# Kernel optimization log

Hardware: AMD Instinct MI355X
Metric: run time of the kernel (lower is better)

## Reference

```python
import jax, jax.numpy as jnp
import numpy as np


def _conv(x, w, padding):
    # x: (N,H,W,Cin), w: (kh,kw,Cin,Cout)
    return jax.lax.conv_general_dilated(x, w, (1, 1), padding,
                                        dimension_numbers=('NHWC', 'HWIO', 'NHWC'))


def _hard_sigmoid(x):
    # Keras default recurrent_activation for ConvLSTM2D
    return jnp.clip(0.2 * x + 0.5, 0.0, 1.0)


def _convlstm(x, Wx, Wh, b):
    # x: (B,T,H,W,Cin); Wx: (3,3,Cin,4F) input conv (VALID, as Keras padding default);
    # Wh: (3,3,F,4F) recurrent conv (SAME, Keras always); b: (4F,). Gate order i,f,c,o.
    B, T, H, W, C = x.shape
    F = Wh.shape[2]
    # Input convolutions are state-independent: compute for all timesteps at once.
    xg = _conv(x.reshape(B * T, H, W, C), Wx, 'VALID') + b  # (B*T, H-2, W-2, 4F)
    Ho, Wo = xg.shape[1], xg.shape[2]
    xg = xg.reshape(B, T, Ho, Wo, 4 * F).transpose(1, 0, 2, 3, 4)  # (T,B,Ho,Wo,4F)
    h0 = jnp.zeros((B, Ho, Wo, F), x.dtype)

    def step(carry, g_t):
        h, c = carry
        g = g_t + _conv(h, Wh, 'SAME')
        i, f, cc, o = jnp.split(g, 4, axis=-1)
        c = _hard_sigmoid(f) * c + _hard_sigmoid(i) * jnp.tanh(cc)
        h = _hard_sigmoid(o) * jnp.tanh(c)
        return (h, c), h

    _, hs = jax.lax.scan(step, (h0, h0), xg)  # hs: (T,B,Ho,Wo,F)
    return hs.transpose(1, 0, 2, 3, 4)


def _maxpool_hw(x):
    # MaxPooling3D pool=(1,2,2), stride=pool, padding='same' on (B,T,H,W,C)
    return jax.lax.reduce_window(x, -jnp.inf, jax.lax.max,
                                 (1, 1, 2, 2, 1), (1, 1, 2, 2, 1), 'SAME')


def setup_inputs() -> dict:
    key = jax.random.key(0)
    ks = jax.random.split(key, 11)
    B, T, H, W, C = 32, 24, 128, 128, 3
    NUM_CLASSES = 50
    FLAT = 24 * 7 * 7 * 16  # = 18816, see shape trace
    p = lambda k, s: (jax.random.normal(k, s, jnp.float32) * 0.05)
    return {
        'x': jax.random.normal(ks[0], (B, T, H, W, C), jnp.float32),
        'Wx1': p(ks[1], (3, 3, 3, 16)),  'Wh1': p(ks[2], (3, 3, 4, 16)),  'b1': jnp.zeros((16,), jnp.float32),
        'Wx2': p(ks[3], (3, 3, 4, 32)),  'Wh2': p(ks[4], (3, 3, 8, 32)),  'b2': jnp.zeros((32,), jnp.float32),
        'Wx3': p(ks[5], (3, 3, 8, 48)),  'Wh3': p(ks[6], (3, 3, 12, 48)), 'b3': jnp.zeros((48,), jnp.float32),
        'Wx4': p(ks[7], (3, 3, 12, 64)), 'Wh4': p(ks[8], (3, 3, 16, 64)), 'b4': jnp.zeros((64,), jnp.float32),
        'Wd': p(ks[9], (FLAT, NUM_CLASSES)), 'bd': jnp.zeros((NUM_CLASSES,), jnp.float32),
    }


def reference(x, Wx1, Wh1, b1, Wx2, Wh2, b2, Wx3, Wh3, b3, Wx4, Wh4, b4, Wd, bd):
    # Dropout layers are identity at inference.
    x = _maxpool_hw(_convlstm(x, Wx1, Wh1, b1))
    x = _maxpool_hw(_convlstm(x, Wx2, Wh2, b2))
    x = _maxpool_hw(_convlstm(x, Wx3, Wh3, b3))
    x = _maxpool_hw(_convlstm(x, Wx4, Wh4, b4))
    x = x.reshape(x.shape[0], -1)  # Keras Flatten: row-major over (T,H,W,C)
    return jax.nn.softmax(x @ Wd + bd, axis=-1)
```

## Files before the change

kernel.cpp:

```cpp
#include <hip/hip_runtime.h>
#include <math.h>


static __device__ __forceinline__ float hsig(float x) {
    return fminf(fmaxf(fmaf(0.2f, x, 0.5f), 0.0f), 1.0f);
}
static __device__ __forceinline__ float ftanh(float x) {
    float e = __builtin_amdgcn_exp2f(x * 2.88539008177792681f);
    return 1.0f - 2.0f * __builtin_amdgcn_rcpf(e + 1.0f);
}

constexpr int H1SL = 32 * 126 * 126 * 4;
constexpr int H2SL = 32 * 61 * 61 * 8;
constexpr int H3SL = 32 * 29 * 29 * 12;
constexpr int H4SL = 32 * 13 * 13 * 16;
constexpr size_t O_H1 = 0;
constexpr size_t O_H2 = O_H1 + 2 * (size_t)H1SL;
constexpr size_t O_H3 = O_H2 + 2 * (size_t)H2SL;
constexpr size_t O_H4 = O_H3 + 2 * (size_t)H3SL;
constexpr size_t O_C1 = O_H4 + 2 * (size_t)H4SL;
constexpr size_t O_C2 = O_C1 + (size_t)H1SL;
constexpr size_t O_C3 = O_C2 + (size_t)H2SL;
constexpr size_t O_C4 = O_C3 + (size_t)H3SL;
constexpr size_t O_P1 = O_C4 + (size_t)H4SL;
constexpr size_t O_P2 = O_P1 + (size_t)(768 * 63 * 63 * 4);
constexpr size_t O_P3 = O_P2 + (size_t)(768 * 31 * 31 * 8);
constexpr size_t O_P4 = O_P3 + (size_t)(768 * 15 * 15 * 12);
constexpr size_t O_DP = O_P4 + (size_t)(768 * 7 * 7 * 16);

__host__ __device__ static inline int role_blocks(int r, int s) {
    int t;
    switch (r) {
    case 0: t = s - 8; return (t >= 0 && t < 24) ? 32   : 0;
    case 1: t = s - 6; return (t >= 0 && t < 24) ? 85   : 0;
    case 2: t = s - 4; return (t >= 0 && t < 24) ? 421  : 0;
    case 3: t = s;     return (t >= 0 && t < 24) ? 993  : 0;
    case 4: t = s - 2; return (t >= 0 && t < 24) ? 1861 : 0;
    case 5: t = s - 1; return (t >= 0 && t < 24) ? 497  : 0;
    case 6: t = s - 3; return (t >= 0 && t < 24) ? 121  : 0;
    case 7: t = s - 5; return (t >= 0 && t < 24) ? 29   : 0;
    case 8: t = s - 7; return (t >= 0 && t < 24) ? 7    : 0;
    }
    return 0;
}
constexpr int NSTAGES = 32;

__device__ __forceinline__
void step_pair_d(const float* __restrict__ P,
                 const float* __restrict__ Wx,
                 const float* __restrict__ Wh,
                 const float* __restrict__ bias,
                 const float* __restrict__ h_prev,
                 float* __restrict__ h_cur,
                 float* __restrict__ cbuf,
                 int t, int lb)
{
    constexpr int CIN = 3, F = 4, HIN = 128, WIN = 128;
    constexpr int B = 32, T = 24, HO = 126, WO = 126, G = 16;
    constexpr int XP = WO / 2;
    constexpr int NPAIR = B * HO * XP;
    const int id = lb * 256 + (int)threadIdx.x;
    if (id >= NPAIR) return;
    const int xp = id % XP;
    const int yy = (id / XP) % HO;
    const int b  = id / (XP * HO);
    const int x0 = 2 * xp;

    float acc[2][4][F];
    #pragma unroll
    for (int u = 0; u < 2; ++u)
        #pragma unroll
        for (int g = 0; g < 4; ++g)
            #pragma unroll
            for (int f = 0; f < F; ++f)
                acc[u][g][f] = bias[g * F + f];

    const float* Pt = P + (size_t)(b * T + t) * HIN * WIN * CIN;
    #pragma unroll
    for (int ky = 0; ky < 3; ++ky) {
        const float* prow = Pt + ((size_t)(yy + ky) * WIN + x0) * CIN;
        float pv[4 * CIN];
        #pragma unroll
        for (int j = 0; j < 2 * CIN; ++j) {
            float2 v2 = reinterpret_cast<const float2*>(prow)[j];
            pv[2 * j] = v2.x; pv[2 * j + 1] = v2.y;
        }
        #pragma unroll
        for (int dx = 0; dx < 4; ++dx)
            #pragma unroll
            for (int ci = 0; ci < CIN; ++ci) {
                const float v = pv[dx * CIN + ci];
                #pragma unroll
                for (int u = 0; u < 2; ++u) {
                    const int kx = dx - u;
                    if (kx >= 0 && kx <= 2) {
                        const float* wr =
                            Wx + (size_t)((ky * 3 + kx) * CIN + ci) * G;
                        #pragma unroll
                        for (int g = 0; g < 4; ++g)
                            #pragma unroll
                            for (int f = 0; f < F; ++f)
                                acc[u][g][f] = fmaf(v, wr[g * F + f], acc[u][g][f]);
                    }
                }
            }
    }

    if (t > 0) {
        #pragma unroll
        for (int ky = 0; ky < 3; ++ky) {
            const int hy = yy + ky - 1;
            if (hy < 0 || hy >= HO) continue;
            const float* hrow = h_prev + ((size_t)b * HO + hy) * WO * F;
            #pragma unroll
            for (int dx = 0; dx < 4; ++dx) {
                const int hx = x0 - 1 + dx;
                if (dx == 0 && x0 == 0) continue;
                if (dx == 3 && hx >= WO) continue;
                const float4* h4 =
                    reinterpret_cast<const float4*>(hrow + (size_t)hx * F);
                float hv[F];
                #pragma unroll
                for (int j = 0; j < F / 4; ++j) {
                    float4 v4 = h4[j];
                    hv[4*j] = v4.x; hv[4*j+1] = v4.y;
                    hv[4*j+2] = v4.z; hv[4*j+3] = v4.w;
                }
                #pragma unroll
                for (int ci = 0; ci < F; ++ci) {
                    const float v = hv[ci];
                    #pragma unroll
                    for (int u = 0; u < 2; ++u) {
                        const int kx = dx - u;
                        if (kx >= 0 && kx <= 2) {
                            const float* wr =
                                Wh + (size_t)((ky * 3 + kx) * F + ci) * G;
                            #pragma unroll
                            for (int g = 0; g < 4; ++g)
                                #pragma unroll
                                for (int f = 0; f < F; ++f)
                                    acc[u][g][f] =
                                        fmaf(v, wr[g * F + f], acc[u][g][f]);
                        }
                    }
                }
            }
        }
    }

    #pragma unroll
    for (int u = 0; u < 2; ++u) {
        const size_t pix = ((size_t)b * HO + yy) * WO + (x0 + u);
        float cn[F], ho[F];
        float* cp = cbuf + pix * F;
        #pragma unroll
        for (int j = 0; j < F / 4; ++j) {
            float4 c4 = (t > 0) ? reinterpret_cast<float4*>(cp)[j]
                                : make_float4(0.f, 0.f, 0.f, 0.f);
            float cold[4] = {c4.x, c4.y, c4.z, c4.w};
            #pragma unroll
            for (int v = 0; v < 4; ++v) {
                const int f = 4 * j + v;
                const float ig = hsig(acc[u][0][f]), fg = hsig(acc[u][1][f]);
                const float cc = ftanh(acc[u][2][f]), og = hsig(acc[u][3][f]);
                cn[f] = fmaf(fg, cold[v], ig * cc);
                ho[f] = og * ftanh(cn[f]);
            }
            reinterpret_cast<float4*>(cp)[j] =
                make_float4(cn[4*j], cn[4*j+1], cn[4*j+2], cn[4*j+3]);
        }
        float* hp = h_cur + pix * F;
        #pragma unroll
        for (int j = 0; j < F / 4; ++j)
            reinterpret_cast<float4*>(hp)[j] =
                make_float4(ho[4*j], ho[4*j+1], ho[4*j+2], ho[4*j+3]);
    }
}

template<int CIN, int F, int HIN, int WIN>
__device__ __forceinline__
void step_split_d(const float* __restrict__ P,
                  const float* __restrict__ Wx,
                  const float* __restrict__ Wh,
                  const float* __restrict__ bias,
                  const float* __restrict__ h_prev,
                  float* __restrict__ h_cur,
                  float* __restrict__ cbuf,
                  int t, int lb, float* __restrict__ gb)
{
    constexpr int B = 32, T = 24, HO = HIN - 2, WO = WIN - 2, G = 4 * F;
    constexpr int NPIX = B * HO * WO;
    const int tid = (int)threadIdx.x, lane = tid & 63;
    const int w = __builtin_amdgcn_readfirstlane(tid >> 6);
    const int pix = lb * 64 + lane;
    const int pp  = (pix < NPIX) ? pix : NPIX - 1;
    const int sp  = pp % (HO * WO);
    const int b   = pp / (HO * WO);
    const int xx  = sp % WO, yy = sp / WO;

    float acc[F];
    #pragma unroll
    for (int f = 0; f < F; ++f) acc[f] = bias[w * F + f];

    const float* Pt = P + (size_t)(b * T + t) * HIN * WIN * CIN;
    #pragma unroll
    for (int ky = 0; ky < 3; ++ky) {
        #pragma unroll
        for (int kx = 0; kx < 3; ++kx) {
            const float* prow = Pt + ((size_t)(yy + ky) * WIN + (xx + kx)) * CIN;
            float pv[CIN];
            #pragma unroll
            for (int j = 0; j < CIN / 4; ++j) {
                float4 v4 = reinterpret_cast<const float4*>(prow)[j];
                pv[4*j] = v4.x; pv[4*j+1] = v4.y; pv[4*j+2] = v4.z; pv[4*j+3] = v4.w;
            }
            #pragma unroll
            for (int ci = 0; ci < CIN; ++ci) {
                const float v = pv[ci];
                const float* wr = Wx + (size_t)((ky * 3 + kx) * CIN + ci) * G + w * F;
                #pragma unroll
                for (int f = 0; f < F; ++f)
                    acc[f] = fmaf(v, wr[f], acc[f]);
            }
        }
    }

    if (t > 0) {
        const float* Hp = h_prev + (size_t)b * HO * WO * F;
        #pragma unroll
        for (int ky = 0; ky < 3; ++ky) {
            const int hy = yy + ky - 1;
            if (hy < 0 || hy >= HO) continue;
            #pragma unroll
            for (int kx = 0; kx < 3; ++kx) {
                const int hx = xx + kx - 1;
                if (hx < 0 || hx >= WO) continue;
                const float4* h4 = reinterpret_cast<const float4*>(
                    Hp + ((size_t)hy * WO + hx) * F);
                float hv[F];
                #pragma unroll
                for (int j = 0; j < F / 4; ++j) {
                    float4 v4 = h4[j];
                    hv[4*j] = v4.x; hv[4*j+1] = v4.y; hv[4*j+2] = v4.z; hv[4*j+3] = v4.w;
                }
                #pragma unroll
                for (int ci = 0; ci < F; ++ci) {
                    const float v = hv[ci];
                    const float* wr = Wh + (size_t)((ky * 3 + kx) * F + ci) * G + w * F;
                    #pragma unroll
                    for (int f = 0; f < F; ++f)
                        acc[f] = fmaf(v, wr[f], acc[f]);
                }
            }
        }
    }

    #pragma unroll
    for (int f = 0; f < F; ++f) gb[w * (64 * F) + lane * F + f] = acc[f];
    __syncthreads();

    #pragma unroll
    for (int r2 = 0; r2 < F / 4; ++r2) {
        const int it = r2 * 256 + tid;
        const int pl = it / F, fo = it % F;
        const int pix2 = lb * 64 + pl;
        if (pix2 < NPIX) {
            const float ig = hsig(gb[0 * (64*F) + it]), fg = hsig(gb[1 * (64*F) + it]);
            const float cc = ftanh(gb[2 * (64*F) + it]), og = hsig(gb[3 * (64*F) + it]);
            const size_t cix = (size_t)pix2 * F + fo;
            const float cold = (t > 0) ? cbuf[cix] : 0.0f;
            const float cnw = fmaf(fg, cold, ig * cc);
            cbuf[cix] = cnw;
            h_cur[cix] = og * ftanh(cnw);
        }
    }
}

template<int C, int H, int W, int HP, int WP>
__device__ __forceinline__
void pool_slice_d(const float* __restrict__ h,
                  float* __restrict__ outF,
                  int t, int lb)
{
    constexpr int B = 32, T = 24;
    const int idx = lb * 256 + (int)threadIdx.x;
    if (idx >= B * HP * WP) return;
    const int xo = idx % WP;
    const int yo = (idx / WP) % HP;
    const int b  = idx / (WP * HP);
    const int y0 = 2 * yo, x0 = 2 * xo;
    const float* p = h + ((size_t)(b * H + y0) * W + x0) * C;
    float m[C];
    #pragma unroll
    for (int j = 0; j < C / 4; ++j) {
        float4 v = reinterpret_cast<const float4*>(p)[j];
        m[4*j] = v.x; m[4*j+1] = v.y; m[4*j+2] = v.z; m[4*j+3] = v.w;
    }
    if (x0 + 1 < W) {
        const float4* q = reinterpret_cast<const float4*>(p + C);
        #pragma unroll
        for (int j = 0; j < C / 4; ++j) {
            float4 v = q[j];
            m[4*j]   = fmaxf(m[4*j],   v.x); m[4*j+1] = fmaxf(m[4*j+1], v.y);
            m[4*j+2] = fmaxf(m[4*j+2], v.z); m[4*j+3] = fmaxf(m[4*j+3], v.w);
        }
    }
    if (y0 + 1 < H) {
        const float4* q = reinterpret_cast<const float4*>(p + (size_t)W * C);
        #pragma unroll
        for (int j = 0; j < C / 4; ++j) {
            float4 v = q[j];
            m[4*j]   = fmaxf(m[4*j],   v.x); m[4*j+1] = fmaxf(m[4*j+1], v.y);
            m[4*j+2] = fmaxf(m[4*j+2], v.z); m[4*j+3] = fmaxf(m[4*j+3], v.w);
        }
        if (x0 + 1 < W) {
            const float4* q2 = reinterpret_cast<const float4*>(p + (size_t)(W + 1) * C);
            #pragma unroll
            for (int j = 0; j < C / 4; ++j) {
                float4 v = q2[j];
                m[4*j]   = fmaxf(m[4*j],   v.x); m[4*j+1] = fmaxf(m[4*j+1], v.y);
                m[4*j+2] = fmaxf(m[4*j+2], v.z); m[4*j+3] = fmaxf(m[4*j+3], v.w);
            }
        }
    }
    float* o = outF + ((size_t)(b * T + t) * HP * WP + (size_t)yo * WP + xo) * C;
    #pragma unroll
    for (int j = 0; j < C / 4; ++j)
        reinterpret_cast<float4*>(o)[j] =
            make_float4(m[4*j], m[4*j+1], m[4*j+2], m[4*j+3]);
}

__device__ __forceinline__
void dense_partial_d(const float* __restrict__ X, const float* __restrict__ Wd,
                     float* __restrict__ part, int ch, int lb,
                     float* __restrict__ red)
{
    constexpr int FLAT = 18816, K = 50, NC = 24, CHUNK = FLAT / NC;
    const int b = lb;
    const int tid = (int)threadIdx.x, lane = tid & 63, wv = tid >> 6;
    const float* xp = X + (size_t)b * FLAT;
    const int i0 = ch * CHUNK + wv * (CHUNK / 4);
    float a0 = 0.f, a1 = 0.f, a2 = 0.f, a3 = 0.f;
    if (lane < K) {
        #pragma unroll 4
        for (int i = i0; i < i0 + CHUNK / 4; i += 4) {
            a0 = fmaf(xp[i + 0], Wd[(size_t)(i + 0) * K + lane], a0);
            a1 = fmaf(xp[i + 1], Wd[(size_t)(i + 1) * K + lane], a1);
            a2 = fmaf(xp[i + 2], Wd[(size_t)(i + 2) * K + lane], a2);
            a3 = fmaf(xp[i + 3], Wd[(size_t)(i + 3) * K + lane], a3);
        }
    }
    red[tid] = (a0 + a1) + (a2 + a3);
    __syncthreads();
    if (tid < 64 && lane < K)
        part[((size_t)b * NC + ch) * K + lane]
            = red[tid] + red[tid + 64] + red[tid + 128] + red[tid + 192];
}

__global__ __launch_bounds__(256)
void pipe_k(const float* __restrict__ x,
            const float* __restrict__ Wx1, const float* __restrict__ Wh1, const float* __restrict__ b1,
            const float* __restrict__ Wx2, const float* __restrict__ Wh2, const float* __restrict__ b2,
            const float* __restrict__ Wx3, const float* __restrict__ Wh3, const float* __restrict__ b3,
            const float* __restrict__ Wx4, const float* __restrict__ Wh4, const float* __restrict__ b4,
            const float* __restrict__ Wd,
            float* __restrict__ ws, int s)
{
    float* h1 = ws + O_H1;  float* h2 = ws + O_H2;
    float* h3 = ws + O_H3;  float* h4 = ws + O_H4;
    float* c1 = ws + O_C1;  float* c2 = ws + O_C2;
    float* c3 = ws + O_C3;  float* c4 = ws + O_C4;
    float* p1 = ws + O_P1;  float* p2 = ws + O_P2;
    float* p3 = ws + O_P3;  float* p4 = ws + O_P4;
    float* dp = ws + O_DP;

    __shared__ float gb[4 * 64 * 16];

    int bid = (int)blockIdx.x, r = 0, cum = 0;
    for (; r < 9; ++r) {
        int n = role_blocks(r, s);
        if (bid < cum + n) break;
        cum += n;
    }
    const int lb = bid - cum;

    switch (r) {
    case 0: { const int ch = s - 8;
        dense_partial_d(p4, Wd, dp, ch, lb, gb); } break;
    case 1: { const int t = s - 6;
        step_split_d<12, 16, 15, 15>(p3, Wx4, Wh4, b4,
            h4 + ((t - 1) & 1) * (size_t)H4SL, h4 + (t & 1) * (size_t)H4SL,
            c4, t, lb, gb); } break;
    case 2: { const int t = s - 4;
        step_split_d<8, 12, 31, 31>(p2, Wx3, Wh3, b3,
            h3 + ((t - 1) & 1) * (size_t)H3SL, h3 + (t & 1) * (size_t)H3SL,
            c3, t, lb, gb); } break;
    case 3: { const int t = s;
        step_pair_d(x, Wx1, Wh1, b1,
            h1 + ((t - 1) & 1) * (size_t)H1SL, h1 + (t & 1) * (size_t)H1SL,
            c1, t, lb); } break;
    case 4: { const int t = s - 2;
        step_split_d<4, 8, 63, 63>(p1, Wx2, Wh2, b2,
            h2 + ((t - 1) & 1) * (size_t)H2SL, h2 + (t & 1) * (size_t)H2SL,
            c2, t, lb, gb); } break;
    case 5: { const int t = s - 1;
        pool_slice_d<4, 126, 126, 63, 63>(h1 + (t & 1) * (size_t)H1SL, p1, t, lb); } break;
    case 6: { const int t = s - 3;
        pool_slice_d<8, 61, 61, 31, 31>(h2 + (t & 1) * (size_t)H2SL, p2, t, lb); } break;
    case 7: { const int t = s - 5;
        pool_slice_d<12, 29, 29, 15, 15>(h3 + (t & 1) * (size_t)H3SL, p3, t, lb); } break;
    case 8: { const int t = s - 7;
        pool_slice_d<16, 13, 13, 7, 7>(h4 + (t & 1) * (size_t)H4SL, p4, t, lb); } break;
    }
}

__global__ __launch_bounds__(64)
void dense_finish_k(const float* __restrict__ part, const float* __restrict__ bd,
                    float* __restrict__ out)
{
    constexpr int K = 50, NC = 24;
    const int b = blockIdx.x, lane = threadIdx.x;
    float v = -INFINITY;
    if (lane < K) {
        v = bd[lane];
        #pragma unroll
        for (int c = 0; c < NC; ++c)
            v += part[((size_t)b * NC + c) * K + lane];
    }
    float m = v;
    #pragma unroll
    for (int off = 32; off > 0; off >>= 1) m = fmaxf(m, __shfl_xor(m, off));
    float e = (lane < K) ? __expf(v - m) : 0.0f;
    float sgm = e;
    #pragma unroll
    for (int off = 32; off > 0; off >>= 1) sgm += __shfl_xor(sgm, off);
    if (lane < K) out[(size_t)b * K + lane] = e / sgm;
}

extern "C" void kernel_launch(void* const* d_in, const int* in_sizes, int n_in,
                              void* d_out, int out_size, void* d_ws, size_t ws_size,
                              hipStream_t stream)
{
    const float* x   = (const float*)d_in[0];
    const float* Wx1 = (const float*)d_in[1];
    const float* Wh1 = (const float*)d_in[2];
    const float* b1  = (const float*)d_in[3];
    const float* Wx2 = (const float*)d_in[4];
    const float* Wh2 = (const float*)d_in[5];
    const float* b2  = (const float*)d_in[6];
    const float* Wx3 = (const float*)d_in[7];
    const float* Wh3 = (const float*)d_in[8];
    const float* b3  = (const float*)d_in[9];
    const float* Wx4 = (const float*)d_in[10];
    const float* Wh4 = (const float*)d_in[11];
    const float* b4  = (const float*)d_in[12];
    const float* Wd  = (const float*)d_in[13];
    const float* bd  = (const float*)d_in[14];
    float* out = (float*)d_out;
    float* ws  = (float*)d_ws;

    for (int s = 0; s < NSTAGES; ++s) {
        int nb = 0;
        for (int r = 0; r < 9; ++r) nb += role_blocks(r, s);
        pipe_k<<<nb, 256, 0, stream>>>(x,
                                       Wx1, Wh1, b1, Wx2, Wh2, b2,
                                       Wx3, Wh3, b3, Wx4, Wh4, b4,
                                       Wd, ws, s);
    }
    dense_finish_k<<<32, 64, 0, stream>>>(ws + O_DP, bd, out);
}
```

Measured before the change: 1.179 ms.

## Fuse max-pooling into ConvLSTM steps via atomic float max and shorten pipeline

```diff
diff --git a/kernel.cpp b/kernel.cpp
--- a/kernel.cpp
+++ b/kernel.cpp
@@ -8,6 +8,12 @@
 static __device__ __forceinline__ float ftanh(float x) {
     float e = __builtin_amdgcn_exp2f(x * 2.88539008177792681f);
     return 1.0f - 2.0f * __builtin_amdgcn_rcpf(e + 1.0f);
+}
+
+static __device__ __forceinline__ void atomic_fmax(float* a, float v) {
+    if (__float_as_uint(v) == 0x80000000u) v = 0.0f;
+    if (v >= 0.0f) atomicMax((int*)a, __float_as_int(v));
+    else           atomicMin((unsigned int*)a, __float_as_uint(v));
 }
 
 constexpr int H1SL = 32 * 126 * 126 * 4;
@@ -27,23 +33,30 @@
 constexpr size_t O_P3 = O_P2 + (size_t)(768 * 31 * 31 * 8);
 constexpr size_t O_P4 = O_P3 + (size_t)(768 * 15 * 15 * 12);
 constexpr size_t O_DP = O_P4 + (size_t)(768 * 7 * 7 * 16);
+constexpr size_t NPOOLF = O_DP - O_P1;
 
 __host__ __device__ static inline int role_blocks(int r, int s) {
     int t;
     switch (r) {
-    case 0: t = s - 8; return (t >= 0 && t < 24) ? 32   : 0;
-    case 1: t = s - 6; return (t >= 0 && t < 24) ? 85   : 0;
-    case 2: t = s - 4; return (t >= 0 && t < 24) ? 421  : 0;
+    case 0: t = s - 4; return (t >= 0 && t < 24) ? 32   : 0;
+    case 1: t = s - 3; return (t >= 0 && t < 24) ? 85   : 0;
+    case 2: t = s - 2; return (t >= 0 && t < 24) ? 421  : 0;
     case 3: t = s;     return (t >= 0 && t < 24) ? 993  : 0;
-    case 4: t = s - 2; return (t >= 0 && t < 24) ? 1861 : 0;
-    case 5: t = s - 1; return (t >= 0 && t < 24) ? 497  : 0;
-    case 6: t = s - 3; return (t >= 0 && t < 24) ? 121  : 0;
-    case 7: t = s - 5; return (t >= 0 && t < 24) ? 29   : 0;
-    case 8: t = s - 7; return (t >= 0 && t < 24) ? 7    : 0;
+    case 4: t = s - 1; return (t >= 0 && t < 24) ? 1861 : 0;
     }
     return 0;
 }
-constexpr int NSTAGES = 32;
+constexpr int NSTAGES = 28;
+
+__global__ __launch_bounds__(256)
+void init_pools_k(float* __restrict__ p)
+{
+    const size_t stride = (size_t)gridDim.x * 256 * 4;
+    for (size_t i = ((size_t)blockIdx.x * 256 + threadIdx.x) * 4;
+         i + 3 < NPOOLF; i += stride)
+        *reinterpret_cast<float4*>(p + i) =
+            make_float4(-INFINITY, -INFINITY, -INFINITY, -INFINITY);
+}
 
 __device__ __forceinline__
 void step_pair_d(const float* __restrict__ P,
@@ -53,6 +66,7 @@
                  const float* __restrict__ h_prev,
                  float* __restrict__ h_cur,
                  float* __restrict__ cbuf,
+                 float* __restrict__ pool,
                  int t, int lb)
 {
     constexpr int CIN = 3, F = 4, HIN = 128, WIN = 128;
@@ -148,10 +162,11 @@
         }
     }
 
+    float hov[2][F];
     #pragma unroll
     for (int u = 0; u < 2; ++u) {
         const size_t pix = ((size_t)b * HO + yy) * WO + (x0 + u);
-        float cn[F], ho[F];
+        float cn[F];
         float* cp = cbuf + pix * F;
         #pragma unroll
         for (int j = 0; j < F / 4; ++j) {
@@ -164,7 +179,7 @@
                 const float ig = hsig(acc[u][0][f]), fg = hsig(acc[u][1][f]);
                 const float cc = ftanh(acc[u][2][f]), og = hsig(acc[u][3][f]);
                 cn[f] = fmaf(fg, cold[v], ig * cc);
-                ho[f] = og * ftanh(cn[f]);
+                hov[u][f] = og * ftanh(cn[f]);
             }
             reinterpret_cast<float4*>(cp)[j] =
                 make_float4(cn[4*j], cn[4*j+1], cn[4*j+2], cn[4*j+3]);
@@ -173,8 +188,13 @@
         #pragma unroll
         for (int j = 0; j < F / 4; ++j)
             reinterpret_cast<float4*>(hp)[j] =
-                make_float4(ho[4*j], ho[4*j+1], ho[4*j+2], ho[4*j+3]);
-    }
+                make_float4(hov[u][4*j], hov[u][4*j+1], hov[u][4*j+2], hov[u][4*j+3]);
+    }
+
+    float* pc = pool + (((size_t)(b * T + t) * 63 + (yy >> 1)) * 63 + xp) * F;
+    #pragma unroll
+    for (int f = 0; f < F; ++f)
+        atomic_fmax(pc + f, fmaxf(hov[0][f], hov[1][f]));
 }
 
 template<int CIN, int F, int HIN, int WIN>
@@ -186,9 +206,11 @@
                   const float* __restrict__ h_prev,
                   float* __restrict__ h_cur,
                   float* __restrict__ cbuf,
+                  float* __restrict__ pool,
                   int t, int lb, float* __restrict__ gb)
 {
     constexpr int B = 32, T = 24, HO = HIN - 2, WO = WIN - 2, G = 4 * F;
+    constexpr int HP = (HO + 1) / 2, WP = (WO + 1) / 2;
     constexpr int NPIX = B * HO * WO;
     const int tid = (int)threadIdx.x, lane = tid & 63;
     const int w = __builtin_amdgcn_readfirstlane(tid >> 6);
@@ -271,63 +293,15 @@
             const float cold = (t > 0) ? cbuf[cix] : 0.0f;
             const float cnw = fmaf(fg, cold, ig * cc);
             cbuf[cix] = cnw;
-            h_cur[cix] = og * ftanh(cnw);
-        }
-    }
-}
-
-template<int C, int H, int W, int HP, int WP>
-__device__ __forceinline__
-void pool_slice_d(const float* __restrict__ h,
-                  float* __restrict__ outF,
-                  int t, int lb)
-{
-    constexpr int B = 32, T = 24;
-    const int idx = lb * 256 + (int)threadIdx.x;
-    if (idx >= B * HP * WP) return;
-    const int xo = idx % WP;
-    const int yo = (idx / WP) % HP;
-    const int b  = idx / (WP * HP);
-    const int y0 = 2 * yo, x0 = 2 * xo;
-    const float* p = h + ((size_t)(b * H + y0) * W + x0) * C;
-    float m[C];
-    #pragma unroll
-    for (int j = 0; j < C / 4; ++j) {
-        float4 v = reinterpret_cast<const float4*>(p)[j];
-        m[4*j] = v.x; m[4*j+1] = v.y; m[4*j+2] = v.z; m[4*j+3] = v.w;
-    }
-    if (x0 + 1 < W) {
-        const float4* q = reinterpret_cast<const float4*>(p + C);
-        #pragma unroll
-        for (int j = 0; j < C / 4; ++j) {
-            float4 v = q[j];
-            m[4*j]   = fmaxf(m[4*j],   v.x); m[4*j+1] = fmaxf(m[4*j+1], v.y);
-            m[4*j+2] = fmaxf(m[4*j+2], v.z); m[4*j+3] = fmaxf(m[4*j+3], v.w);
-        }
-    }
-    if (y0 + 1 < H) {
-        const float4* q = reinterpret_cast<const float4*>(p + (size_t)W * C);
-        #pragma unroll
-        for (int j = 0; j < C / 4; ++j) {
-            float4 v = q[j];
-            m[4*j]   = fmaxf(m[4*j],   v.x); m[4*j+1] = fmaxf(m[4*j+1], v.y);
-            m[4*j+2] = fmaxf(m[4*j+2], v.z); m[4*j+3] = fmaxf(m[4*j+3], v.w);
-        }
-        if (x0 + 1 < W) {
-            const float4* q2 = reinterpret_cast<const float4*>(p + (size_t)(W + 1) * C);
-            #pragma unroll
-            for (int j = 0; j < C / 4; ++j) {
-                float4 v = q2[j];
-                m[4*j]   = fmaxf(m[4*j],   v.x); m[4*j+1] = fmaxf(m[4*j+1], v.y);
-                m[4*j+2] = fmaxf(m[4*j+2], v.z); m[4*j+3] = fmaxf(m[4*j+3], v.w);
-            }
-        }
-    }
-    float* o = outF + ((size_t)(b * T + t) * HP * WP + (size_t)yo * WP + xo) * C;
-    #pragma unroll
-    for (int j = 0; j < C / 4; ++j)
-        reinterpret_cast<float4*>(o)[j] =
-            make_float4(m[4*j], m[4*j+1], m[4*j+2], m[4*j+3]);
+            const float hval = og * ftanh(cnw);
+            h_cur[cix] = hval;
+            const int sp2 = pix2 % (HO * WO);
+            const int b2  = pix2 / (HO * WO);
+            const int xx2 = sp2 % WO, yy2 = sp2 / WO;
+            atomic_fmax(pool + (((size_t)(b2 * T + t) * HP + (yy2 >> 1)) * WP
+                                + (xx2 >> 1)) * F + fo, hval);
+        }
+    }
 }
 
 __device__ __forceinline__
@@ -377,7 +351,7 @@
     __shared__ float gb[4 * 64 * 16];
 
     int bid = (int)blockIdx.x, r = 0, cum = 0;
-    for (; r < 9; ++r) {
+    for (; r < 5; ++r) {
         int n = role_blocks(r, s);
         if (bid < cum + n) break;
         cum += n;
@@ -385,32 +359,24 @@
     const int lb = bid - cum;
 
     switch (r) {
-    case 0: { const int ch = s - 8;
+    case 0: { const int ch = s - 4;
         dense_partial_d(p4, Wd, dp, ch, lb, gb); } break;
-    case 1: { const int t = s - 6;
+    case 1: { const int t = s - 3;
         step_split_d<12, 16, 15, 15>(p3, Wx4, Wh4, b4,
             h4 + ((t - 1) & 1) * (size_t)H4SL, h4 + (t & 1) * (size_t)H4SL,
-            c4, t, lb, gb); } break;
-    case 2: { const int t = s - 4;
+            c4, p4, t, lb, gb); } break;
+    case 2: { const int t = s - 2;
         step_split_d<8, 12, 31, 31>(p2, Wx3, Wh3, b3,
             h3 + ((t - 1) & 1) * (size_t)H3SL, h3 + (t & 1) * (size_t)H3SL,
-            c3, t, lb, gb); } break;
+            c3, p3, t, lb, gb); } break;
     case 3: { const int t = s;
         step_pair_d(x, Wx1, Wh1, b1,
             h1 + ((t - 1) & 1) * (size_t)H1SL, h1 + (t & 1) * (size_t)H1SL,
-            c1, t, lb); } break;
-    case 4: { const int t = s - 2;
+            c1, p1, t, lb); } break;
+    case 4: { const int t = s - 1;
         step_split_d<4, 8, 63, 63>(p1, Wx2, Wh2, b2,
             h2 + ((t - 1) & 1) * (size_t)H2SL, h2 + (t & 1) * (size_t)H2SL,
-            c2, t, lb, gb); } break;
-    case 5: { const int t = s - 1;
-        pool_slice_d<4, 126, 126, 63, 63>(h1 + (t & 1) * (size_t)H1SL, p1, t, lb); } break;
-    case 6: { const int t = s - 3;
-        pool_slice_d<8, 61, 61, 31, 31>(h2 + (t & 1) * (size_t)H2SL, p2, t, lb); } break;
-    case 7: { const int t = s - 5;
-        pool_slice_d<12, 29, 29, 15, 15>(h3 + (t & 1) * (size_t)H3SL, p3, t, lb); } break;
-    case 8: { const int t = s - 7;
-        pool_slice_d<16, 13, 13, 7, 7>(h4 + (t & 1) * (size_t)H4SL, p4, t, lb); } break;
+            c2, p2, t, lb, gb); } break;
     }
 }
 
@@ -459,9 +425,11 @@
     float* out = (float*)d_out;
     float* ws  = (float*)d_ws;
 
+    init_pools_k<<<2048, 256, 0, stream>>>(ws + O_P1);
+
     for (int s = 0; s < NSTAGES; ++s) {
         int nb = 0;
-        for (int r = 0; r < 9; ++r) nb += role_blocks(r, s);
+        for (int r = 0; r < 5; ++r) nb += role_blocks(r, s);
         pipe_k<<<nb, 256, 0, stream>>>(x,
                                        Wx1, Wh1, b1, Wx2, Wh2, b2,
                                        Wx3, Wh3, b3, Wx4, Wh4, b4,
```

New measurement: 1.451 ms. 1.23x slower.

## Split gate channels across waves so each thread finishes its own cell update

Applied to the files above, without the earlier changes.

```diff
diff --git a/kernel.cpp b/kernel.cpp
--- a/kernel.cpp
+++ b/kernel.cpp
@@ -179,28 +179,33 @@
 
 template<int CIN, int F, int HIN, int WIN>
 __device__ __forceinline__
-void step_split_d(const float* __restrict__ P,
-                  const float* __restrict__ Wx,
-                  const float* __restrict__ Wh,
-                  const float* __restrict__ bias,
-                  const float* __restrict__ h_prev,
-                  float* __restrict__ h_cur,
-                  float* __restrict__ cbuf,
-                  int t, int lb, float* __restrict__ gb)
+void step_csplit_d(const float* __restrict__ P,
+                   const float* __restrict__ Wx,
+                   const float* __restrict__ Wh,
+                   const float* __restrict__ bias,
+                   const float* __restrict__ h_prev,
+                   float* __restrict__ h_cur,
+                   float* __restrict__ cbuf,
+                   int t, int lb)
 {
     constexpr int B = 32, T = 24, HO = HIN - 2, WO = WIN - 2, G = 4 * F;
+    constexpr int FH = F / 4;
     constexpr int NPIX = B * HO * WO;
     const int tid = (int)threadIdx.x, lane = tid & 63;
     const int w = __builtin_amdgcn_readfirstlane(tid >> 6);
     const int pix = lb * 64 + lane;
-    const int pp  = (pix < NPIX) ? pix : NPIX - 1;
+    const bool live = (pix < NPIX);
+    const int pp  = live ? pix : NPIX - 1;
     const int sp  = pp % (HO * WO);
     const int b   = pp / (HO * WO);
     const int xx  = sp % WO, yy = sp / WO;
 
-    float acc[F];
-    #pragma unroll
-    for (int f = 0; f < F; ++f) acc[f] = bias[w * F + f];
+    float acc[4][FH];
+    #pragma unroll
+    for (int g = 0; g < 4; ++g)
+        #pragma unroll
+        for (int f = 0; f < FH; ++f)
+            acc[g][f] = bias[g * F + w * FH + f];
 
     const float* Pt = P + (size_t)(b * T + t) * HIN * WIN * CIN;
     #pragma unroll
@@ -217,10 +222,13 @@
             #pragma unroll
             for (int ci = 0; ci < CIN; ++ci) {
                 const float v = pv[ci];
-                const float* wr = Wx + (size_t)((ky * 3 + kx) * CIN + ci) * G + w * F;
-                #pragma unroll
-                for (int f = 0; f < F; ++f)
-                    acc[f] = fmaf(v, wr[f], acc[f]);
+                const float* wr =
+                    Wx + (size_t)((ky * 3 + kx) * CIN + ci) * G + w * FH;
+                #pragma unroll
+                for (int g = 0; g < 4; ++g)
+                    #pragma unroll
+                    for (int f = 0; f < FH; ++f)
+                        acc[g][f] = fmaf(v, wr[g * F + f], acc[g][f]);
             }
         }
     }
@@ -246,32 +254,28 @@
                 #pragma unroll
                 for (int ci = 0; ci < F; ++ci) {
                     const float v = hv[ci];
-                    const float* wr = Wh + (size_t)((ky * 3 + kx) * F + ci) * G + w * F;
+                    const float* wr =
+                        Wh + (size_t)((ky * 3 + kx) * F + ci) * G + w * FH;
                     #pragma unroll
-                    for (int f = 0; f < F; ++f)
-                        acc[f] = fmaf(v, wr[f], acc[f]);
+                    for (int g = 0; g < 4; ++g)
+                        #pragma unroll
+                        for (int f = 0; f < FH; ++f)
+                            acc[g][f] = fmaf(v, wr[g * F + f], acc[g][f]);
                 }
             }
         }
     }
 
-    #pragma unroll
-    for (int f = 0; f < F; ++f) gb[w * (64 * F) + lane * F + f] = acc[f];
-    __syncthreads();
-
-    #pragma unroll
-    for (int r2 = 0; r2 < F / 4; ++r2) {
-        const int it = r2 * 256 + tid;
-        const int pl = it / F, fo = it % F;
-        const int pix2 = lb * 64 + pl;
-        if (pix2 < NPIX) {
-            const float ig = hsig(gb[0 * (64*F) + it]), fg = hsig(gb[1 * (64*F) + it]);
-            const float cc = ftanh(gb[2 * (64*F) + it]), og = hsig(gb[3 * (64*F) + it]);
-            const size_t cix = (size_t)pix2 * F + fo;
-            const float cold = (t > 0) ? cbuf[cix] : 0.0f;
+    if (live) {
+        const size_t base = (size_t)pix * F + w * FH;
+        #pragma unroll
+        for (int f = 0; f < FH; ++f) {
+            const float ig = hsig(acc[0][f]), fg = hsig(acc[1][f]);
+            const float cc = ftanh(acc[2][f]), og = hsig(acc[3][f]);
+            const float cold = (t > 0) ? cbuf[base + f] : 0.0f;
             const float cnw = fmaf(fg, cold, ig * cc);
-            cbuf[cix] = cnw;
-            h_cur[cix] = og * ftanh(cnw);
+            cbuf[base + f] = cnw;
+            h_cur[base + f] = og * ftanh(cnw);
         }
     }
 }
@@ -374,7 +378,7 @@
     float* p3 = ws + O_P3;  float* p4 = ws + O_P4;
     float* dp = ws + O_DP;
 
-    __shared__ float gb[4 * 64 * 16];
+    __shared__ float red[256];
 
     int bid = (int)blockIdx.x, r = 0, cum = 0;
     for (; r < 9; ++r) {
@@ -386,23 +390,23 @@
 
     switch (r) {
     case 0: { const int ch = s - 8;
-        dense_partial_d(p4, Wd, dp, ch, lb, gb); } break;
+        dense_partial_d(p4, Wd, dp, ch, lb, red); } break;
     case 1: { const int t = s - 6;
-        step_split_d<12, 16, 15, 15>(p3, Wx4, Wh4, b4,
+        step_csplit_d<12, 16, 15, 15>(p3, Wx4, Wh4, b4,
             h4 + ((t - 1) & 1) * (size_t)H4SL, h4 + (t & 1) * (size_t)H4SL,
-            c4, t, lb, gb); } break;
+            c4, t, lb); } break;
     case 2: { const int t = s - 4;
-        step_split_d<8, 12, 31, 31>(p2, Wx3, Wh3, b3,
+        step_csplit_d<8, 12, 31, 31>(p2, Wx3, Wh3, b3,
             h3 + ((t - 1) & 1) * (size_t)H3SL, h3 + (t & 1) * (size_t)H3SL,
-            c3, t, lb, gb); } break;
+            c3, t, lb); } break;
     case 3: { const int t = s;
         step_pair_d(x, Wx1, Wh1, b1,
             h1 + ((t - 1) & 1) * (size_t)H1SL, h1 + (t & 1) * (size_t)H1SL,
             c1, t, lb); } break;
     case 4: { const int t = s - 2;
-        step_split_d<4, 8, 63, 63>(p1, Wx2, Wh2, b2,
+        step_csplit_d<4, 8, 63, 63>(p1, Wx2, Wh2, b2,
             h2 + ((t - 1) & 1) * (size_t)H2SL, h2 + (t & 1) * (size_t)H2SL,
-            c2, t, lb, gb); } break;
+            c2, t, lb); } break;
     case 5: { const int t = s - 1;
         pool_slice_d<4, 126, 126, 63, 63>(h1 + (t & 1) * (size_t)H1SL, p1, t, lb); } break;
     case 6: { const int t = s - 3;
```

Measured after the change: 1.842 ms. +56.2%, slower.
